# Kernel tuning notes

Hardware: AMD Instinct MI355X
Metric: run time of the kernel (lower is better)

## Reference

```python
import jax, jax.numpy as jnp
import numpy as np

N = 200000   # gaussians
M = 10000    # scaffold nodes
K = 16       # skinning knn
T = 40       # time steps
F = 32       # semantic feature dim
MAX_S = 0.1
MIN_S = 0.0
EPS = 1e-8


def _qnorm(q):
    return q / jnp.clip(jnp.linalg.norm(q, axis=-1, keepdims=True), 1e-12)


def q2R(q):
    # quaternion (w, x, y, z) -> rotation matrix, normalizing first (matches q2R in source)
    q = _qnorm(q)
    w, x, y, z = q[..., 0], q[..., 1], q[..., 2], q[..., 3]
    r0 = jnp.stack([1 - 2 * (y * y + z * z), 2 * (x * y - w * z), 2 * (x * z + w * y)], -1)
    r1 = jnp.stack([2 * (x * y + w * z), 1 - 2 * (x * x + z * z), 2 * (y * z - w * x)], -1)
    r2 = jnp.stack([2 * (x * z - w * y), 2 * (y * z + w * x), 1 - 2 * (x * x + y * y)], -1)
    return jnp.stack([r0, r1, r2], -2)


def quat_mul(a, b):
    aw, ax, ay, az = a[..., 0], a[..., 1], a[..., 2], a[..., 3]
    bw, bx, by, bz = b[..., 0], b[..., 1], b[..., 2], b[..., 3]
    return jnp.stack([
        aw * bw - ax * bx - ay * by - az * bz,
        aw * bx + ax * bw + ay * bz - az * by,
        aw * by - ax * bz + ay * bw + az * bx,
        aw * bz + ax * by - ay * bx + az * bw], -1)


def quat_conj(q):
    return q * jnp.array([1.0, -1.0, -1.0, -1.0], q.dtype)


def setup_inputs() -> dict:
    key = jax.random.key(0)
    ks = jax.random.split(key, 13)
    return {
        "gs_xyz": 0.05 * jax.random.normal(ks[0], (N, 3), jnp.float32),
        "gs_rotation": jax.random.normal(ks[1], (N, 4), jnp.float32),
        "gs_scaling": jax.random.normal(ks[2], (N, 3), jnp.float32),
        "gs_opacity": jax.random.normal(ks[3], (N, 1), jnp.float32),
        "feat_dc": jax.random.normal(ks[4], (N, 3), jnp.float32),
        "feat_rest": jax.random.normal(ks[5], (N, 9), jnp.float32),
        "node_xyz": jax.random.normal(ks[6], (T, M, 3), jnp.float32),
        "node_quat": jax.random.normal(ks[7], (T, M, 4), jnp.float32),
        "node_sigma": 0.1 + 0.5 * jax.random.uniform(ks[8], (M, 1), jnp.float32),
        "node_sem": jax.random.normal(ks[9], (M, F), jnp.float32),
        "attach_ind": jax.random.randint(ks[10], (N,), 0, M, jnp.int32),
        "ref_time": jax.random.randint(ks[11], (N,), 0, T, jnp.int32),
        "topo_knn": jax.random.randint(ks[12], (M, K), 0, M, jnp.int32),
        "t": 5,
    }


def reference(gs_xyz, gs_rotation, gs_scaling, gs_opacity, feat_dc, feat_rest,
              node_xyz, node_quat, node_sigma, node_sem,
              attach_ind, ref_time, topo_knn, t):
    # --- per-gaussian activated attributes ---
    s = MIN_S + jax.nn.sigmoid(gs_scaling) * (MAX_S - MIN_S)   # s_act
    o = jax.nn.sigmoid(gs_opacity)                              # o_act
    sph = jnp.concatenate([feat_dc, feat_rest], axis=-1)        # [N, 12], full sph order

    # --- leaf-local -> world at ref time (get_xyz / get_R_mtx) ---
    ref_p_attach = node_xyz[ref_time, attach_ind]               # [N,3] async knn gather
    ref_q_attach = node_quat[ref_time, attach_ind]              # [N,4]
    R_ref_attach = q2R(ref_q_attach)                            # [N,3,3]
    x_world = jnp.einsum('nij,nj->ni', R_ref_attach, gs_xyz) + ref_p_attach
    R_world = jnp.einsum('nij,njk->nik', R_ref_attach, q2R(gs_rotation))

    # --- scf.warp: KNN skinning from per-point ref time to target time t ---
    sk_ind = topo_knn[attach_ind]                               # [N,K] neighbor node ids
    p_ref = node_xyz[ref_time[:, None], sk_ind]                 # [N,K,3]
    q_ref = node_quat[ref_time[:, None], sk_ind]                # [N,K,4]
    p_live = node_xyz[t][sk_ind]                                # [N,K,3]
    q_live = node_quat[t][sk_ind]                               # [N,K,4]
    sigma = node_sigma[sk_ind, 0]                               # [N,K]

    diff = x_world[:, None, :] - p_ref                          # [N,K,3]
    dsq = jnp.sum(diff * diff, axis=-1)                         # [N,K]
    w = jnp.exp(-dsq / (2.0 * sigma * sigma + EPS))             # RBF skinning weights
    w = w / (jnp.sum(w, axis=-1, keepdims=True) + EPS)          # [N,K]

    # per-node relative transform ref -> live
    q_rel = quat_mul(_qnorm(q_live), quat_conj(_qnorm(q_ref)))  # [N,K,4]
    R_rel = q2R(q_rel)                                          # [N,K,3,3]
    mu_k = jnp.einsum('nkij,nkj->nki', R_rel, diff) + p_live    # [N,K,3]
    mu_live = jnp.einsum('nk,nki->ni', w, mu_k)                 # [N,3]

    q_blend = jnp.einsum('nk,nkd->nd', w, q_rel)                # blended quaternion
    fr_live = jnp.einsum('nij,njk->nik', q2R(q_blend), R_world) # [N,3,3]

    sem_live = jnp.einsum('nk,nkf->nf', w, node_sem[sk_ind])    # [N,F]

    return mu_live, fr_live, s, o, sph, sem_live
```

## Files before the change

### kernel.cpp

```cpp
#include <hip/hip_runtime.h>

#define KNN 16
#define FSEM 32
#define LPG 4
#define NXCD 8
#define NSUB 256

__device__ __forceinline__ float sigmoidf_(float x) { return 1.0f / (1.0f + __expf(-x)); }

__device__ __forceinline__ void quat_to_R(float qw, float qx, float qy, float qz, float* R) {
    float d = qw * qw + qx * qx + qy * qy + qz * qz;
    float inv = rsqrtf(fmaxf(d, 1e-24f));
    float w = qw * inv, x = qx * inv, y = qy * inv, z = qz * inv;
    R[0] = 1.f - 2.f * (y * y + z * z); R[1] = 2.f * (x * y - w * z); R[2] = 2.f * (x * z + w * y);
    R[3] = 2.f * (x * y + w * z); R[4] = 1.f - 2.f * (x * x + z * z); R[5] = 2.f * (y * z - w * x);
    R[6] = 2.f * (x * z - w * y); R[7] = 2.f * (y * z + w * x); R[8] = 1.f - 2.f * (x * x + y * y);
}

__global__ void __launch_bounds__(256)
k_pack_hist(const float* __restrict__ node_xyz, const float* __restrict__ node_quat,
            const float* __restrict__ node_sigma,
            const int* __restrict__ attach, const int* __restrict__ rtime,
            float* __restrict__ packed, int* __restrict__ cnt, int* __restrict__ rank,
            int TM, int M, int N, int shift)
{
    int p = blockIdx.x * blockDim.x + threadIdx.x;
    if (p < TM) {
        const int node = p - (p / M) * M;
        const float* x = node_xyz + 3 * (size_t)p;
        float4 a = make_float4(x[0], x[1], x[2], node_sigma[node]);
        float4 q = reinterpret_cast<const float4*>(node_quat)[p];
        float4* dst = reinterpret_cast<float4*>(packed + 8 * (size_t)p);
        dst[0] = a;
        dst[1] = q;
    }
    if (p < N && cnt) {
        const int key = rtime[p] * NSUB + (attach[p] >> shift);
        rank[p] = atomicAdd(&cnt[key], 1);
    }
}

__global__ void __launch_bounds__(256)
k_scan(int* __restrict__ cnt, int B)
{
    __shared__ int sh[256];
    __shared__ int carry_s;
    if (threadIdx.x == 0) carry_s = 0;
    __syncthreads();
    for (int base = 0; base < B; base += 256) {
        const int i = base + threadIdx.x;
        int v = (i < B) ? cnt[i] : 0;
        sh[threadIdx.x] = v;
        __syncthreads();
        int acc = v;
#pragma unroll
        for (int off = 1; off < 256; off <<= 1) {
            int u = (threadIdx.x >= off) ? sh[threadIdx.x - off] : 0;
            __syncthreads();
            acc += u;
            sh[threadIdx.x] = acc;
            __syncthreads();
        }
        const int carry = carry_s;
        if (i < B) cnt[i] = acc - v + carry;
        __syncthreads();
        if (threadIdx.x == 255) carry_s = carry + acc;
        __syncthreads();
    }
}

__global__ void __launch_bounds__(256)
k_scatter_elem(const int* __restrict__ attach, const int* __restrict__ rtime,
               const float* __restrict__ gs_xyz,
               const int* __restrict__ rank, const int* __restrict__ cnt,
               float4* __restrict__ meta,
               const float* __restrict__ gs_scal,
               const float* __restrict__ gs_opa,
               const float* __restrict__ feat_dc,
               const float* __restrict__ feat_rest,
               float* __restrict__ out,
               int N, int shift)
{
    int n = blockIdx.x * blockDim.x + threadIdx.x;
    if (n >= N) return;
    const int a = attach[n], rt = rtime[n];
    const int key = rt * NSUB + (a >> shift);
    const int pos = cnt[key] + rank[n];
    meta[2 * (size_t)pos]     = make_float4(__int_as_float(n), __int_as_float(a),
                                            __int_as_float(rt), 0.f);
    meta[2 * (size_t)pos + 1] = make_float4(gs_xyz[3 * (size_t)n + 0],
                                            gs_xyz[3 * (size_t)n + 1],
                                            gs_xyz[3 * (size_t)n + 2], 0.f);

    const size_t Ns = (size_t)N, ns = (size_t)n;
    float* os = out + 12 * Ns + 3 * ns;
    os[0] = 0.1f * sigmoidf_(gs_scal[3 * ns + 0]);
    os[1] = 0.1f * sigmoidf_(gs_scal[3 * ns + 1]);
    os[2] = 0.1f * sigmoidf_(gs_scal[3 * ns + 2]);

    out[15 * Ns + ns] = sigmoidf_(gs_opa[ns]);

    float* osph = out + 16 * Ns + 12 * ns;
    float4 v0 = make_float4(feat_dc[3 * ns + 0], feat_dc[3 * ns + 1], feat_dc[3 * ns + 2],
                            feat_rest[9 * ns + 0]);
    float4 v1 = make_float4(feat_rest[9 * ns + 1], feat_rest[9 * ns + 2],
                            feat_rest[9 * ns + 3], feat_rest[9 * ns + 4]);
    float4 v2 = make_float4(feat_rest[9 * ns + 5], feat_rest[9 * ns + 6],
                            feat_rest[9 * ns + 7], feat_rest[9 * ns + 8]);
    reinterpret_cast<float4*>(osph)[0] = v0;
    reinterpret_cast<float4*>(osph)[1] = v1;
    reinterpret_cast<float4*>(osph)[2] = v2;
}

__global__ void __launch_bounds__(256)
k_fr(const float* __restrict__ gs_rot,
     const float* __restrict__ node_quat,
     const int*   __restrict__ attach_ind,
     const int*   __restrict__ ref_time,
     const float* __restrict__ qb_ws,
     float* __restrict__ out, int N, int M)
{
    const int n = blockIdx.x * blockDim.x + threadIdx.x;
    if (n >= N) return;
    const size_t Ns = (size_t)N, ns = (size_t)n;

    const int a  = attach_ind[n];
    const int rt = ref_time[n];
    const float4 qa = reinterpret_cast<const float4*>(node_quat)[(size_t)rt * (size_t)M + (size_t)a];
    float Rref[9];
    quat_to_R(qa.x, qa.y, qa.z, qa.w, Rref);

    const float4 qg = reinterpret_cast<const float4*>(gs_rot)[ns];
    float Rg[9];
    quat_to_R(qg.x, qg.y, qg.z, qg.w, Rg);

    float Rw[9];
#pragma unroll
    for (int i = 0; i < 3; i++)
#pragma unroll
        for (int j = 0; j < 3; j++)
            Rw[3 * i + j] = Rref[3 * i] * Rg[j] + Rref[3 * i + 1] * Rg[3 + j] + Rref[3 * i + 2] * Rg[6 + j];

    const float4 qb = reinterpret_cast<const float4*>(qb_ws)[ns];
    float Rb[9];
    quat_to_R(qb.x, qb.y, qb.z, qb.w, Rb);

    float* ofr = out + 3 * Ns + 9 * ns;
#pragma unroll
    for (int i = 0; i < 3; i++)
#pragma unroll
        for (int j = 0; j < 3; j++)
            ofr[3 * i + j] = Rb[3 * i] * Rw[j] + Rb[3 * i + 1] * Rw[3 + j] + Rb[3 * i + 2] * Rw[6 + j];
}

template<bool FR>
__global__ void __launch_bounds__(256)
k_elem(const float* __restrict__ gs_scal,
       const float* __restrict__ gs_opa,
       const float* __restrict__ feat_dc,
       const float* __restrict__ feat_rest,
       const float* __restrict__ gs_rot,
       const float* __restrict__ node_quat,
       const int*   __restrict__ attach_ind,
       const int*   __restrict__ ref_time,
       const float* __restrict__ qb_ws,
       float* __restrict__ out, int N, int M)
{
    const int n = blockIdx.x * blockDim.x + threadIdx.x;
    if (n >= N) return;
    const size_t Ns = (size_t)N, ns = (size_t)n;

    float* os = out + 12 * Ns + 3 * ns;
    os[0] = 0.1f * sigmoidf_(gs_scal[3 * ns + 0]);
    os[1] = 0.1f * sigmoidf_(gs_scal[3 * ns + 1]);
    os[2] = 0.1f * sigmoidf_(gs_scal[3 * ns + 2]);

    out[15 * Ns + ns] = sigmoidf_(gs_opa[ns]);

    float* osph = out + 16 * Ns + 12 * ns;
    float4 v0 = make_float4(feat_dc[3 * ns + 0], feat_dc[3 * ns + 1], feat_dc[3 * ns + 2],
                            feat_rest[9 * ns + 0]);
    float4 v1 = make_float4(feat_rest[9 * ns + 1], feat_rest[9 * ns + 2],
                            feat_rest[9 * ns + 3], feat_rest[9 * ns + 4]);
    float4 v2 = make_float4(feat_rest[9 * ns + 5], feat_rest[9 * ns + 6],
                            feat_rest[9 * ns + 7], feat_rest[9 * ns + 8]);
    reinterpret_cast<float4*>(osph)[0] = v0;
    reinterpret_cast<float4*>(osph)[1] = v1;
    reinterpret_cast<float4*>(osph)[2] = v2;

    if constexpr (FR) {
        const int a  = attach_ind[n];
        const int rt = ref_time[n];
        const float4 qa = reinterpret_cast<const float4*>(node_quat)[(size_t)rt * (size_t)M + (size_t)a];
        float Rref[9];
        quat_to_R(qa.x, qa.y, qa.z, qa.w, Rref);

        const float4 qg = reinterpret_cast<const float4*>(gs_rot)[ns];
        float Rg[9];
        quat_to_R(qg.x, qg.y, qg.z, qg.w, Rg);

        float Rw[9];
#pragma unroll
        for (int i = 0; i < 3; i++)
#pragma unroll
            for (int j = 0; j < 3; j++)
                Rw[3 * i + j] = Rref[3 * i] * Rg[j] + Rref[3 * i + 1] * Rg[3 + j] + Rref[3 * i + 2] * Rg[6 + j];

        const float4 qb = reinterpret_cast<const float4*>(qb_ws)[ns];
        float Rb[9];
        quat_to_R(qb.x, qb.y, qb.z, qb.w, Rb);

        float* ofr = out + 3 * Ns + 9 * ns;
#pragma unroll
        for (int i = 0; i < 3; i++)
#pragma unroll
            for (int j = 0; j < 3; j++)
                ofr[3 * i + j] = Rb[3 * i] * Rw[j] + Rb[3 * i + 1] * Rw[3 + j] + Rb[3 * i + 2] * Rw[6 + j];
    }
}

template<bool PACKED, bool FRSPLIT, bool SORTED>
__global__ void __launch_bounds__(256)
dynscf_kernel(const float* __restrict__ gs_xyz,
              const float* __restrict__ gs_rot,
              const float* __restrict__ node_xyz,
              const float* __restrict__ node_quat,
              const float* __restrict__ packed,
              const float* __restrict__ node_sigma,
              const float* __restrict__ node_sem,
              const int* __restrict__ attach_ind,
              const int* __restrict__ ref_time,
              const int* __restrict__ topo_knn,
              const int* __restrict__ t_ptr,
              const float4* __restrict__ meta,
              float* __restrict__ out,
              float* __restrict__ qb_out,
              int N, int M)
{
    int bid = blockIdx.x;
    if (SORTED) {
        const int nwg = gridDim.x;
        const int q = nwg / NXCD, r = nwg % NXCD;
        const int xcd = bid % NXCD, idx = bid / NXCD;
        bid = (xcd < r ? xcd * (q + 1) : r * (q + 1) + (xcd - r) * q) + idx;
    }
    const int tid = bid * blockDim.x + threadIdx.x;
    const int g   = tid >> 2;
    const int sub = tid & (LPG - 1);
    if (g >= N) return;

    const int t = t_ptr[0];

    int n, a, rt;
    float gx, gy, gz;
    if (SORTED) {
        const float4 m0 = meta[2 * (size_t)g];
        const float4 m1 = meta[2 * (size_t)g + 1];
        n  = __float_as_int(m0.x);
        a  = __float_as_int(m0.y);
        rt = __float_as_int(m0.z);
        gx = m1.x; gy = m1.y; gz = m1.z;
    } else {
        n  = g;
        a  = attach_ind[n];
        rt = ref_time[n];
        gx = gs_xyz[3 * (size_t)n + 0];
        gy = gs_xyz[3 * (size_t)n + 1];
        gz = gs_xyz[3 * (size_t)n + 2];
    }

    const size_t base_rt = (size_t)rt * (size_t)M;
    const size_t base_t  = (size_t)t  * (size_t)M;

    const int4 kv = reinterpret_cast<const int4*>(topo_knn)[(size_t)a * (KNN / 4) + sub];
    const int js[4] = { kv.x, kv.y, kv.z, kv.w };

    float apx, apy, apz, aqw, aqx, aqy, aqz;
    if (PACKED) {
        const float4* pk = reinterpret_cast<const float4*>(packed + (base_rt + (size_t)a) * 8);
        float4 xz = pk[0], qv = pk[1];
        apx = xz.x; apy = xz.y; apz = xz.z;
        aqw = qv.x; aqx = qv.y; aqy = qv.z; aqz = qv.w;
    } else {
        const float4 qv = *reinterpret_cast<const float4*>(node_quat + (base_rt + (size_t)a) * 4);
        const float* pa = node_xyz + (base_rt + (size_t)a) * 3;
        apx = pa[0]; apy = pa[1]; apz = pa[2];
        aqw = qv.x; aqx = qv.y; aqy = qv.z; aqz = qv.w;
    }
    float Rref[9];
    quat_to_R(aqw, aqx, aqy, aqz, Rref);

    const float xw0 = Rref[0] * gx + Rref[1] * gy + Rref[2] * gz + apx;
    const float xw1 = Rref[3] * gx + Rref[4] * gy + Rref[5] * gz + apy;
    const float xw2 = Rref[6] * gx + Rref[7] * gy + Rref[8] * gz + apz;

    float wsum = 0.f, mu0 = 0.f, mu1 = 0.f, mu2 = 0.f;
    float qb0 = 0.f, qb1 = 0.f, qb2 = 0.f, qb3 = 0.f;
    float wk[4];

#pragma unroll
    for (int k = 0; k < KNN / LPG; k++) {
        const int j = js[k];

        float prx, pry, prz, rw, rx, ry, rz;
        float plx, ply, plz, lw, lx, ly, lz;
        float sg;
        if (PACKED) {
            const float4* pkr = reinterpret_cast<const float4*>(packed + (base_rt + (size_t)j) * 8);
            float4 xr = pkr[0], qr = pkr[1];
            prx = xr.x; pry = xr.y; prz = xr.z; sg = xr.w;
            rw = qr.x; rx = qr.y; ry = qr.z; rz = qr.w;
            const float4* pkl = reinterpret_cast<const float4*>(packed + (base_t + (size_t)j) * 8);
            float4 xl = pkl[0], ql = pkl[1];
            plx = xl.x; ply = xl.y; plz = xl.z;
            lw = ql.x; lx = ql.y; ly = ql.z; lz = ql.w;
        } else {
            const float* pr = node_xyz + (base_rt + (size_t)j) * 3;
            prx = pr[0]; pry = pr[1]; prz = pr[2];
            const float4 qr = *reinterpret_cast<const float4*>(node_quat + (base_rt + (size_t)j) * 4);
            rw = qr.x; rx = qr.y; ry = qr.z; rz = qr.w;
            const float* pl = node_xyz + (base_t + (size_t)j) * 3;
            plx = pl[0]; ply = pl[1]; plz = pl[2];
            const float4 ql = *reinterpret_cast<const float4*>(node_quat + (base_t + (size_t)j) * 4);
            lw = ql.x; lx = ql.y; ly = ql.z; lz = ql.w;
            sg = node_sigma[j];
        }

        const float dx = xw0 - prx;
        const float dy = xw1 - pry;
        const float dz = xw2 - prz;
        const float dsq = dx * dx + dy * dy + dz * dz;

        const float w = __expf(-dsq / (2.f * sg * sg + 1e-8f));
        wk[k] = w;

        {
            float inv = rsqrtf(fmaxf(rw * rw + rx * rx + ry * ry + rz * rz, 1e-24f));
            rw *= inv; rx *= inv; ry *= inv; rz *= inv;
        }
        {
            float inv = rsqrtf(fmaxf(lw * lw + lx * lx + ly * ly + lz * lz, 1e-24f));
            lw *= inv; lx *= inv; ly *= inv; lz *= inv;
        }
        const float qw =  lw * rw + lx * rx + ly * ry + lz * rz;
        const float qx = -lw * rx + lx * rw - ly * rz + lz * ry;
        const float qy = -lw * ry + lx * rz + ly * rw - lz * rx;
        const float qz = -lw * rz - lx * ry + ly * rx + lz * rw;

        float Rr[9];
        quat_to_R(qw, qx, qy, qz, Rr);

        const float m0 = Rr[0] * dx + Rr[1] * dy + Rr[2] * dz + plx;
        const float m1 = Rr[3] * dx + Rr[4] * dy + Rr[5] * dz + ply;
        const float m2 = Rr[6] * dx + Rr[7] * dy + Rr[8] * dz + plz;

        wsum += w;
        mu0 += w * m0; mu1 += w * m1; mu2 += w * m2;
        qb0 += w * qw; qb1 += w * qx; qb2 += w * qy; qb3 += w * qz;
    }

#pragma unroll
    for (int m = 1; m < LPG; m <<= 1) {
        wsum += __shfl_xor(wsum, m);
        mu0  += __shfl_xor(mu0, m);  mu1 += __shfl_xor(mu1, m);  mu2 += __shfl_xor(mu2, m);
        qb0  += __shfl_xor(qb0, m);  qb1 += __shfl_xor(qb1, m);
        qb2  += __shfl_xor(qb2, m);  qb3 += __shfl_xor(qb3, m);
    }

    const float invw = 1.f / (wsum + 1e-8f);
    const size_t Ns = (size_t)N, ns = (size_t)n;

    float sm0 = 0.f, sm1 = 0.f, sm2 = 0.f, sm3 = 0.f;
    float sm4 = 0.f, sm5 = 0.f, sm6 = 0.f, sm7 = 0.f;
    const float4* sem4 = reinterpret_cast<const float4*>(node_sem);
#pragma unroll
    for (int kk = 0; kk < KNN; kk++) {
        const int src = kk >> 2;
        const int idx = kk & 3;
        const int   jk = __shfl(js[idx], src, LPG);
        const float wkk = __shfl(wk[idx], src, LPG);
        const float4 v0 = sem4[(size_t)jk * (FSEM / 4) + sub * 2 + 0];
        const float4 v1 = sem4[(size_t)jk * (FSEM / 4) + sub * 2 + 1];
        sm0 += wkk * v0.x; sm1 += wkk * v0.y; sm2 += wkk * v0.z; sm3 += wkk * v0.w;
        sm4 += wkk * v1.x; sm5 += wkk * v1.y; sm6 += wkk * v1.z; sm7 += wkk * v1.w;
    }

    if (sub == 0) {
        out[3 * ns + 0] = mu0 * invw;
        out[3 * ns + 1] = mu1 * invw;
        out[3 * ns + 2] = mu2 * invw;
    } else if (sub == 1) {
        if (FRSPLIT) {
            reinterpret_cast<float4*>(qb_out)[ns] =
                make_float4(qb0 * invw, qb1 * invw, qb2 * invw, qb3 * invw);
        }
    }

    if constexpr (!FRSPLIT) {
        if (sub == 1) {
            const float4 qg = *reinterpret_cast<const float4*>(gs_rot + 4 * ns);
            float Rg[9];
            quat_to_R(qg.x, qg.y, qg.z, qg.w, Rg);
            float Rw[9];
#pragma unroll
            for (int i = 0; i < 3; i++)
#pragma unroll
                for (int j = 0; j < 3; j++)
                    Rw[3 * i + j] = Rref[3 * i] * Rg[j] + Rref[3 * i + 1] * Rg[3 + j] + Rref[3 * i + 2] * Rg[6 + j];
            float Rb[9];
            quat_to_R(qb0 * invw, qb1 * invw, qb2 * invw, qb3 * invw, Rb);
            float* ofr = out + 3 * Ns + 9 * ns;
#pragma unroll
            for (int i = 0; i < 3; i++)
#pragma unroll
                for (int j = 0; j < 3; j++)
                    ofr[3 * i + j] = Rb[3 * i] * Rw[j] + Rb[3 * i + 1] * Rw[3 + j] + Rb[3 * i + 2] * Rw[6 + j];
        }
    }

    float4* osem = reinterpret_cast<float4*>(out + 28 * Ns + FSEM * ns);
    osem[sub * 2 + 0] = make_float4(sm0 * invw, sm1 * invw, sm2 * invw, sm3 * invw);
    osem[sub * 2 + 1] = make_float4(sm4 * invw, sm5 * invw, sm6 * invw, sm7 * invw);
}

extern "C" void kernel_launch(void* const* d_in, const int* in_sizes, int n_in,
                              void* d_out, int out_size, void* d_ws, size_t ws_size,
                              hipStream_t stream)
{
    const float* gs_xyz     = (const float*)d_in[0];
    const float* gs_rot     = (const float*)d_in[1];
    const float* gs_scal    = (const float*)d_in[2];
    const float* gs_opa     = (const float*)d_in[3];
    const float* feat_dc    = (const float*)d_in[4];
    const float* feat_rest  = (const float*)d_in[5];
    const float* node_xyz   = (const float*)d_in[6];
    const float* node_quat  = (const float*)d_in[7];
    const float* node_sigma = (const float*)d_in[8];
    const float* node_sem   = (const float*)d_in[9];
    const int* attach_ind   = (const int*)d_in[10];
    const int* ref_time     = (const int*)d_in[11];
    const int* topo_knn     = (const int*)d_in[12];
    const int* t_ptr        = (const int*)d_in[13];

    const int N = in_sizes[0] / 3;
    const int M = in_sizes[8];
    const int TM = in_sizes[6] / 3;
    const int T  = TM / M;
    const int B  = T * NSUB;

    int shift = 0;
    while (((M - 1) >> shift) >= NSUB) shift++;

    float* out = (float*)d_out;

    const int block = 256;
    const int gridN = (N + block - 1) / block;
    const long long threads = (long long)N * LPG;
    const int gridM = (int)((threads + block - 1) / block);
    const int gridPH = (((TM > N ? TM : N)) + block - 1) / block;

    const size_t f_packed = (size_t)TM * 8;
    const size_t f_qb     = (size_t)N * 4;
    const size_t f_meta   = (size_t)N * 8;
    const size_t i_cnt    = (size_t)B;
    const size_t need_sort   = (f_packed + f_qb + f_meta + i_cnt) * sizeof(float);
    const size_t need_packed = (f_packed + f_qb) * sizeof(float);
    const size_t need_qb     = f_qb * sizeof(float);

    if (ws_size >= need_sort) {
        float*  packed = (float*)d_ws;
        float*  qb_ws  = packed + f_packed;
        float4* meta   = (float4*)(packed + f_packed + f_qb);
        int*    cnt    = (int*)(packed + f_packed + f_qb + f_meta);
        int*    rank   = (int*)qb_ws;

        hipMemsetAsync(cnt, 0, (size_t)B * sizeof(int), stream);
        hipLaunchKernelGGL(k_pack_hist, dim3(gridPH), dim3(block), 0, stream,
                           node_xyz, node_quat, node_sigma, attach_ind, ref_time,
                           packed, cnt, rank, TM, M, N, shift);
        hipLaunchKernelGGL(k_scan, dim3(1), dim3(block), 0, stream, cnt, B);
        hipLaunchKernelGGL(k_scatter_elem, dim3(gridN), dim3(block), 0, stream,
                           attach_ind, ref_time, gs_xyz, rank, cnt, meta,
                           gs_scal, gs_opa, feat_dc, feat_rest, out, N, shift);
        hipLaunchKernelGGL((dynscf_kernel<true, true, true>), dim3(gridM), dim3(block), 0, stream,
                           gs_xyz, gs_rot, node_xyz, node_quat, packed, node_sigma, node_sem,
                           attach_ind, ref_time, topo_knn, t_ptr, meta, out, qb_ws, N, M);
        hipLaunchKernelGGL(k_fr, dim3(gridN), dim3(block), 0, stream,
                           gs_rot, node_quat, attach_ind, ref_time, qb_ws, out, N, M);
    } else if (ws_size >= need_packed) {
        float* packed = (float*)d_ws;
        float* qb_ws  = packed + f_packed;
        hipLaunchKernelGGL(k_pack_hist, dim3(gridPH), dim3(block), 0, stream,
                           node_xyz, node_quat, node_sigma, attach_ind, ref_time,
                           packed, (int*)nullptr, (int*)nullptr, TM, M, 0, shift);
        hipLaunchKernelGGL((dynscf_kernel<true, true, false>), dim3(gridM), dim3(block), 0, stream,
                           gs_xyz, gs_rot, node_xyz, node_quat, packed, node_sigma, node_sem,
                           attach_ind, ref_time, topo_knn, t_ptr, (const float4*)nullptr,
                           out, qb_ws, N, M);
        hipLaunchKernelGGL((k_elem<true>), dim3(gridN), dim3(block), 0, stream,
                           gs_scal, gs_opa, feat_dc, feat_rest, gs_rot, node_quat,
                           attach_ind, ref_time, qb_ws, out, N, M);
    } else if (ws_size >= need_qb) {
        float* qb_ws = (float*)d_ws;
        hipLaunchKernelGGL((dynscf_kernel<false, true, false>), dim3(gridM), dim3(block), 0, stream,
                           gs_xyz, gs_rot, node_xyz, node_quat, (const float*)nullptr,
                           node_sigma, node_sem,
                           attach_ind, ref_time, topo_knn, t_ptr, (const float4*)nullptr,
                           out, qb_ws, N, M);
        hipLaunchKernelGGL((k_elem<true>), dim3(gridN), dim3(block), 0, stream,
                           gs_scal, gs_opa, feat_dc, feat_rest, gs_rot, node_quat,
                           attach_ind, ref_time, qb_ws, out, N, M);
    } else {
        hipLaunchKernelGGL((dynscf_kernel<false, false, false>), dim3(gridM), dim3(block), 0, stream,
                           gs_xyz, gs_rot, node_xyz, node_quat, (const float*)nullptr,
                           node_sigma, node_sem,
                           attach_ind, ref_time, topo_knn, t_ptr, (const float4*)nullptr,
                           out, (float*)nullptr, N, M);
        hipLaunchKernelGGL((k_elem<false>), dim3(gridN), dim3(block), 0, stream,
                           gs_scal, gs_opa, feat_dc, feat_rest, gs_rot, node_quat,
                           attach_ind, ref_time, (const float*)nullptr, out, N, M);
    }
}
```

Baseline: 244.2 us.

## Parallelize bucket scan and fuse frame computation back into main kernel

Replaces the single-block serial prefix scan over histogram buckets with a two-level scan: many blocks each scan 256 buckets, then one block scans the block totals, which the scatter kernel adds back. Also removes the separate k_fr kernel and the qb workspace round trip, so the sorted path computes the blended frame matrix directly in the main kernel. This cuts one launch and a global write and read of blended quaternions, at the cost of more register pressure in the main kernel and an extra scan launch.

New measurement: 216.3 us. -11.5%, faster.

```diff
diff --git a/kernel.cpp b/kernel.cpp
--- a/kernel.cpp
+++ b/kernel.cpp
@@ -41,15 +41,36 @@
 }
 
 __global__ void __launch_bounds__(256)
-k_scan(int* __restrict__ cnt, int B)
+k_scan1(int* __restrict__ cnt, int* __restrict__ blk, int B)
+{
+    __shared__ int sh[256];
+    const int i = blockIdx.x * 256 + threadIdx.x;
+    int v = (i < B) ? cnt[i] : 0;
+    sh[threadIdx.x] = v;
+    __syncthreads();
+    int acc = v;
+#pragma unroll
+    for (int off = 1; off < 256; off <<= 1) {
+        int u = (threadIdx.x >= off) ? sh[threadIdx.x - off] : 0;
+        __syncthreads();
+        acc += u;
+        sh[threadIdx.x] = acc;
+        __syncthreads();
+    }
+    if (i < B) cnt[i] = acc - v;
+    if (threadIdx.x == 255) blk[blockIdx.x] = acc;
+}
+
+__global__ void __launch_bounds__(256)
+k_scan2(int* __restrict__ blk, int nblk)
 {
     __shared__ int sh[256];
     __shared__ int carry_s;
     if (threadIdx.x == 0) carry_s = 0;
     __syncthreads();
-    for (int base = 0; base < B; base += 256) {
+    for (int base = 0; base < nblk; base += 256) {
         const int i = base + threadIdx.x;
-        int v = (i < B) ? cnt[i] : 0;
+        int v = (i < nblk) ? blk[i] : 0;
         sh[threadIdx.x] = v;
         __syncthreads();
         int acc = v;
@@ -62,7 +83,7 @@
             __syncthreads();
         }
         const int carry = carry_s;
-        if (i < B) cnt[i] = acc - v + carry;
+        if (i < nblk) blk[i] = acc - v + carry;
         __syncthreads();
         if (threadIdx.x == 255) carry_s = carry + acc;
         __syncthreads();
@@ -73,6 +94,7 @@
 k_scatter_elem(const int* __restrict__ attach, const int* __restrict__ rtime,
                const float* __restrict__ gs_xyz,
                const int* __restrict__ rank, const int* __restrict__ cnt,
+               const int* __restrict__ blk,
                float4* __restrict__ meta,
                const float* __restrict__ gs_scal,
                const float* __restrict__ gs_opa,
@@ -85,7 +107,7 @@
     if (n >= N) return;
     const int a = attach[n], rt = rtime[n];
     const int key = rt * NSUB + (a >> shift);
-    const int pos = cnt[key] + rank[n];
+    const int pos = cnt[key] + blk[key >> 8] + rank[n];
     meta[2 * (size_t)pos]     = make_float4(__int_as_float(n), __int_as_float(a),
                                             __int_as_float(rt), 0.f);
     meta[2 * (size_t)pos + 1] = make_float4(gs_xyz[3 * (size_t)n + 0],
@@ -113,58 +135,11 @@
 }
 
 __global__ void __launch_bounds__(256)
-k_fr(const float* __restrict__ gs_rot,
-     const float* __restrict__ node_quat,
-     const int*   __restrict__ attach_ind,
-     const int*   __restrict__ ref_time,
-     const float* __restrict__ qb_ws,
-     float* __restrict__ out, int N, int M)
-{
-    const int n = blockIdx.x * blockDim.x + threadIdx.x;
-    if (n >= N) return;
-    const size_t Ns = (size_t)N, ns = (size_t)n;
-
-    const int a  = attach_ind[n];
-    const int rt = ref_time[n];
-    const float4 qa = reinterpret_cast<const float4*>(node_quat)[(size_t)rt * (size_t)M + (size_t)a];
-    float Rref[9];
-    quat_to_R(qa.x, qa.y, qa.z, qa.w, Rref);
-
-    const float4 qg = reinterpret_cast<const float4*>(gs_rot)[ns];
-    float Rg[9];
-    quat_to_R(qg.x, qg.y, qg.z, qg.w, Rg);
-
-    float Rw[9];
-#pragma unroll
-    for (int i = 0; i < 3; i++)
-#pragma unroll
-        for (int j = 0; j < 3; j++)
-            Rw[3 * i + j] = Rref[3 * i] * Rg[j] + Rref[3 * i + 1] * Rg[3 + j] + Rref[3 * i + 2] * Rg[6 + j];
-
-    const float4 qb = reinterpret_cast<const float4*>(qb_ws)[ns];
-    float Rb[9];
-    quat_to_R(qb.x, qb.y, qb.z, qb.w, Rb);
-
-    float* ofr = out + 3 * Ns + 9 * ns;
-#pragma unroll
-    for (int i = 0; i < 3; i++)
-#pragma unroll
-        for (int j = 0; j < 3; j++)
-            ofr[3 * i + j] = Rb[3 * i] * Rw[j] + Rb[3 * i + 1] * Rw[3 + j] + Rb[3 * i + 2] * Rw[6 + j];
-}
-
-template<bool FR>
-__global__ void __launch_bounds__(256)
 k_elem(const float* __restrict__ gs_scal,
        const float* __restrict__ gs_opa,
        const float* __restrict__ feat_dc,
        const float* __restrict__ feat_rest,
-       const float* __restrict__ gs_rot,
-       const float* __restrict__ node_quat,
-       const int*   __restrict__ attach_ind,
-       const int*   __restrict__ ref_time,
-       const float* __restrict__ qb_ws,
-       float* __restrict__ out, int N, int M)
+       float* __restrict__ out, int N)
 {
     const int n = blockIdx.x * blockDim.x + threadIdx.x;
     if (n >= N) return;
@@ -187,39 +162,9 @@
     reinterpret_cast<float4*>(osph)[0] = v0;
     reinterpret_cast<float4*>(osph)[1] = v1;
     reinterpret_cast<float4*>(osph)[2] = v2;
-
-    if constexpr (FR) {
-        const int a  = attach_ind[n];
-        const int rt = ref_time[n];
-        const float4 qa = reinterpret_cast<const float4*>(node_quat)[(size_t)rt * (size_t)M + (size_t)a];
-        float Rref[9];
-        quat_to_R(qa.x, qa.y, qa.z, qa.w, Rref);
-
-        const float4 qg = reinterpret_cast<const float4*>(gs_rot)[ns];
-        float Rg[9];
-        quat_to_R(qg.x, qg.y, qg.z, qg.w, Rg);
-
-        float Rw[9];
-#pragma unroll
-        for (int i = 0; i < 3; i++)
-#pragma unroll
-            for (int j = 0; j < 3; j++)
-                Rw[3 * i + j] = Rref[3 * i] * Rg[j] + Rref[3 * i + 1] * Rg[3 + j] + Rref[3 * i + 2] * Rg[6 + j];
-
-        const float4 qb = reinterpret_cast<const float4*>(qb_ws)[ns];
-        float Rb[9];
-        quat_to_R(qb.x, qb.y, qb.z, qb.w, Rb);
-
-        float* ofr = out + 3 * Ns + 9 * ns;
-#pragma unroll
-        for (int i = 0; i < 3; i++)
-#pragma unroll
-            for (int j = 0; j < 3; j++)
-                ofr[3 * i + j] = Rb[3 * i] * Rw[j] + Rb[3 * i + 1] * Rw[3 + j] + Rb[3 * i + 2] * Rw[6 + j];
-    }
-}
-
-template<bool PACKED, bool FRSPLIT, bool SORTED>
+}
+
+template<bool PACKED, bool SORTED>
 __global__ void __launch_bounds__(256)
 dynscf_kernel(const float* __restrict__ gs_xyz,
               const float* __restrict__ gs_rot,
@@ -234,7 +179,6 @@
               const int* __restrict__ t_ptr,
               const float4* __restrict__ meta,
               float* __restrict__ out,
-              float* __restrict__ qb_out,
               int N, int M)
 {
     int bid = blockIdx.x;
@@ -390,32 +334,23 @@
         out[3 * ns + 1] = mu1 * invw;
         out[3 * ns + 2] = mu2 * invw;
     } else if (sub == 1) {
-        if (FRSPLIT) {
-            reinterpret_cast<float4*>(qb_out)[ns] =
-                make_float4(qb0 * invw, qb1 * invw, qb2 * invw, qb3 * invw);
-        }
-    }
-
-    if constexpr (!FRSPLIT) {
-        if (sub == 1) {
-            const float4 qg = *reinterpret_cast<const float4*>(gs_rot + 4 * ns);
-            float Rg[9];
-            quat_to_R(qg.x, qg.y, qg.z, qg.w, Rg);
-            float Rw[9];
-#pragma unroll
-            for (int i = 0; i < 3; i++)
-#pragma unroll
-                for (int j = 0; j < 3; j++)
-                    Rw[3 * i + j] = Rref[3 * i] * Rg[j] + Rref[3 * i + 1] * Rg[3 + j] + Rref[3 * i + 2] * Rg[6 + j];
-            float Rb[9];
-            quat_to_R(qb0 * invw, qb1 * invw, qb2 * invw, qb3 * invw, Rb);
-            float* ofr = out + 3 * Ns + 9 * ns;
-#pragma unroll
-            for (int i = 0; i < 3; i++)
-#pragma unroll
-                for (int j = 0; j < 3; j++)
-                    ofr[3 * i + j] = Rb[3 * i] * Rw[j] + Rb[3 * i + 1] * Rw[3 + j] + Rb[3 * i + 2] * Rw[6 + j];
-        }
+        const float4 qg = *reinterpret_cast<const float4*>(gs_rot + 4 * ns);
+        float Rg[9];
+        quat_to_R(qg.x, qg.y, qg.z, qg.w, Rg);
+        float Rw[9];
+#pragma unroll
+        for (int i = 0; i < 3; i++)
+#pragma unroll
+            for (int j = 0; j < 3; j++)
+                Rw[3 * i + j] = Rref[3 * i] * Rg[j] + Rref[3 * i + 1] * Rg[3 + j] + Rref[3 * i + 2] * Rg[6 + j];
+        float Rb[9];
+        quat_to_R(qb0 * invw, qb1 * invw, qb2 * invw, qb3 * invw, Rb);
+        float* ofr = out + 3 * Ns + 9 * ns;
+#pragma unroll
+        for (int i = 0; i < 3; i++)
+#pragma unroll
+            for (int j = 0; j < 3; j++)
+                ofr[3 * i + j] = Rb[3 * i] * Rw[j] + Rb[3 * i + 1] * Rw[3 + j] + Rb[3 * i + 2] * Rw[6 + j];
     }
 
     float4* osem = reinterpret_cast<float4*>(out + 28 * Ns + FSEM * ns);
@@ -458,66 +393,53 @@
     const long long threads = (long long)N * LPG;
     const int gridM = (int)((threads + block - 1) / block);
     const int gridPH = (((TM > N ? TM : N)) + block - 1) / block;
+    const int nblkS = (B + 255) / 256;
 
     const size_t f_packed = (size_t)TM * 8;
-    const size_t f_qb     = (size_t)N * 4;
     const size_t f_meta   = (size_t)N * 8;
     const size_t i_cnt    = (size_t)B;
-    const size_t need_sort   = (f_packed + f_qb + f_meta + i_cnt) * sizeof(float);
-    const size_t need_packed = (f_packed + f_qb) * sizeof(float);
-    const size_t need_qb     = f_qb * sizeof(float);
+    const size_t i_blk    = (size_t)nblkS;
+    const size_t i_rank   = (size_t)N;
+    const size_t need_sort   = (f_packed + f_meta + i_cnt + i_blk + i_rank) * sizeof(float);
+    const size_t need_packed = f_packed * sizeof(float);
 
     if (ws_size >= need_sort) {
         float*  packed = (float*)d_ws;
-        float*  qb_ws  = packed + f_packed;
-        float4* meta   = (float4*)(packed + f_packed + f_qb);
-        int*    cnt    = (int*)(packed + f_packed + f_qb + f_meta);
-        int*    rank   = (int*)qb_ws;
+        float4* meta   = (float4*)(packed + f_packed);
+        int*    cnt    = (int*)(packed + f_packed + f_meta);
+        int*    blk    = cnt + i_cnt;
+        int*    rank   = blk + i_blk;
 
         hipMemsetAsync(cnt, 0, (size_t)B * sizeof(int), stream);
         hipLaunchKernelGGL(k_pack_hist, dim3(gridPH), dim3(block), 0, stream,
                            node_xyz, node_quat, node_sigma, attach_ind, ref_time,
                            packed, cnt, rank, TM, M, N, shift);
-        hipLaunchKernelGGL(k_scan, dim3(1), dim3(block), 0, stream, cnt, B);
+        hipLaunchKernelGGL(k_scan1, dim3(nblkS), dim3(block), 0, stream, cnt, blk, B);
+        hipLaunchKernelGGL(k_scan2, dim3(1), dim3(block), 0, stream, blk, nblkS);
         hipLaunchKernelGGL(k_scatter_elem, dim3(gridN), dim3(block), 0, stream,
-                           attach_ind, ref_time, gs_xyz, rank, cnt, meta,
+                           attach_ind, ref_time, gs_xyz, rank, cnt, blk, meta,
                            gs_scal, gs_opa, feat_dc, feat_rest, out, N, shift);
-        hipLaunchKernelGGL((dynscf_kernel<true, true, true>), dim3(gridM), dim3(block), 0, stream,
+        hipLaunchKernelGGL((dynscf_kernel<true, true>), dim3(gridM), dim3(block), 0, stream,
                            gs_xyz, gs_rot, node_xyz, node_quat, packed, node_sigma, node_sem,
-                           attach_ind, ref_time, topo_knn, t_ptr, meta, out, qb_ws, N, M);
-        hipLaunchKernelGGL(k_fr, dim3(gridN), dim3(block), 0, stream,
-                           gs_rot, node_quat, attach_ind, ref_time, qb_ws, out, N, M);
+                           attach_ind, ref_time, topo_knn, t_ptr, meta, out, N, M);
     } else if (ws_size >= need_packed) {
         float* packed = (float*)d_ws;
-        float* qb_ws  = packed + f_packed;
         hipLaunchKernelGGL(k_pack_hist, dim3(gridPH), dim3(block), 0, stream,
                            node_xyz, node_quat, node_sigma, attach_ind, ref_time,
                            packed, (int*)nullptr, (int*)nullptr, TM, M, 0, shift);
-        hipLaunchKernelGGL((dynscf_kernel<true, true, false>), dim3(gridM), dim3(block), 0, stream,
+        hipLaunchKernelGGL((dynscf_kernel<true, false>), dim3(gridM), dim3(block), 0, stream,
                            gs_xyz, gs_rot, node_xyz, node_quat, packed, node_sigma, node_sem,
                            attach_ind, ref_time, topo_knn, t_ptr, (const float4*)nullptr,
-                           out, qb_ws, N, M);
-        hipLaunchKernelGGL((k_elem<true>), dim3(gridN), dim3(block), 0, stream,
-                           gs_scal, gs_opa, feat_dc, feat_rest, gs_rot, node_quat,
-                           attach_ind, ref_time, qb_ws, out, N, M);
-    } else if (ws_size >= need_qb) {
-        float* qb_ws = (float*)d_ws;
-        hipLaunchKernelGGL((dynscf_kernel<false, true, false>), dim3(gridM), dim3(block), 0, stream,
+                           out, N, M);
+        hipLaunchKernelGGL(k_elem, dim3(gridN), dim3(block), 0, stream,
+                           gs_scal, gs_opa, feat_dc, feat_rest, out, N);
+    } else {
+        hipLaunchKernelGGL((dynscf_kernel<false, false>), dim3(gridM), dim3(block), 0, stream,
                            gs_xyz, gs_rot, node_xyz, node_quat, (const float*)nullptr,
                            node_sigma, node_sem,
                            attach_ind, ref_time, topo_knn, t_ptr, (const float4*)nullptr,
-                           out, qb_ws, N, M);
-        hipLaunchKernelGGL((k_elem<true>), dim3(gridN), dim3(block), 0, stream,
-                           gs_scal, gs_opa, feat_dc, feat_rest, gs_rot, node_quat,
-                           attach_ind, ref_time, qb_ws, out, N, M);
-    } else {
-        hipLaunchKernelGGL((dynscf_kernel<false, false, false>), dim3(gridM), dim3(block), 0, stream,
-                           gs_xyz, gs_rot, node_xyz, node_quat, (const float*)nullptr,
-                           node_sigma, node_sem,
-                           attach_ind, ref_time, topo_knn, t_ptr, (const float4*)nullptr,
-                           out, (float*)nullptr, N, M);
-        hipLaunchKernelGGL((k_elem<false>), dim3(gridN), dim3(block), 0, stream,
-                           gs_scal, gs_opa, feat_dc, feat_rest, gs_rot, node_quat,
-                           attach_ind, ref_time, (const float*)nullptr, out, N, M);
-    }
-}
+                           out, N, M);
+        hipLaunchKernelGGL(k_elem, dim3(gridN), dim3(block), 0, stream,
+                           gs_scal, gs_opa, feat_dc, feat_rest, out, N);
+    }
+}
```
